# Optimization experiments

Hardware: AMD Instinct MI355X
Metric: run time of the kernel (lower is better)

The kernel has to match this reference:

```python
import jax, jax.numpy as jnp
import numpy as np

B, S, D, H = 2, 2048, 1024, 16
HD = D // H  # head_dim = 64
ROPE_BASE = 10000.0


def setup_inputs() -> dict:
    key = jax.random.key(0)
    ks = jax.random.split(key, 5)
    scale = 1.0 / np.sqrt(D)
    return {
        "x": jax.random.normal(ks[0], (B, S, D), dtype=jnp.float32),
        "Wq": jax.random.normal(ks[1], (D, D), dtype=jnp.float32) * scale,
        "Wk": jax.random.normal(ks[2], (D, D), dtype=jnp.float32) * scale,
        "Wv": jax.random.normal(ks[3], (D, D), dtype=jnp.float32) * scale,
        "Wo": jax.random.normal(ks[4], (D, D), dtype=jnp.float32) * scale,
    }


def _rotate_half(x):
    x1, x2 = x[..., : HD // 2], x[..., HD // 2:]
    return jnp.concatenate((-x2, x1), axis=-1)


def _rope_cos_sin(seq_len):
    inv_freq = 1.0 / (ROPE_BASE ** (jnp.arange(0, HD, 2, dtype=jnp.float32) / HD))
    t = jnp.arange(seq_len, dtype=jnp.float32)
    freqs = jnp.outer(t, inv_freq)          # [S, HD/2]
    emb = jnp.concatenate((freqs, freqs), -1)  # [S, HD]
    return jnp.cos(emb), jnp.sin(emb)


def reference(x, Wq, Wk, Wv, Wo):
    # projections (torch Linear: y = x @ W.T), split heads -> [B, H, S, HD]
    def proj(W):
        return (x @ W.T).reshape(B, S, H, HD).transpose(0, 2, 1, 3)

    q, k, v = proj(Wq), proj(Wk), proj(Wv)

    cos, sin = _rope_cos_sin(S)  # [S, HD] each, broadcast over B, H
    q = q * cos + _rotate_half(q) * sin
    k = k * cos + _rotate_half(k) * sin

    scale = 1.0 / np.sqrt(HD)
    scores = jnp.einsum("bhsd,bhtd->bhst", q, k) * scale  # [B,H,S,S]
    attn = jax.nn.softmax(scores, axis=-1)
    out = jnp.einsum("bhst,bhtd->bhsd", attn, v)           # [B,H,S,HD]
    out = out.transpose(0, 2, 1, 3).reshape(B, S, D)
    return out @ Wo.T
```

## Files before the change

### kernel.cpp

```cpp
#include <hip/hip_runtime.h>
#include <hip/hip_bf16.h>
#include <math.h>
#include <stdint.h>

typedef __bf16 bf16;
typedef __bf16 bf16x8 __attribute__((ext_vector_type(8)));
typedef __bf16 bf16x4 __attribute__((ext_vector_type(4)));
typedef float  f32x4  __attribute__((ext_vector_type(4)));

#define MFMA16(a,b,c) __builtin_amdgcn_mfma_f32_16x16x32_bf16((a),(b),(c),0,0,0)
#define GLOAD_LDS16(g, l) \
  __builtin_amdgcn_global_load_lds((__attribute__((address_space(1))) void*)(g), \
                                   (__attribute__((address_space(3))) void*)(l), 16, 0, 0)

static constexpr int kB  = 2;
static constexpr int kS  = 2048;
static constexpr int kD  = 1024;
static constexpr int kH  = 16;
static constexpr int kHD = 64;
static constexpr int kM  = kB * kS;
static constexpr float kExpC = 0.125f * 1.44269504f;

__global__ void cvt_all(const float* __restrict__ x,
                        const float* __restrict__ wq, const float* __restrict__ wk,
                        const float* __restrict__ wv, const float* __restrict__ wo,
                        bf16* __restrict__ xb,
                        bf16* __restrict__ wqb, bf16* __restrict__ wkb,
                        bf16* __restrict__ wvb, bf16* __restrict__ wob,
                        float2* __restrict__ rtab)
{
  const int i = blockIdx.x * 256 + threadIdx.x;
  const int NX4 = (kM * kD) / 4;
  const int NW4 = (kD * kD) / 4;
  if (i >= NX4 + 4 * NW4) {
    const int idx = i - (NX4 + 4 * NW4);
    const int s = idx >> 5, d = idx & 31;
    const float f = exp2f(-(float)d * 0.4152410118609203f);
    float sn, cs;
    sincosf((float)s * f, &sn, &cs);
    rtab[idx] = make_float2(cs, sn);
    return;
  }
  const float* src; bf16* dst; int off;
  if (i < NX4) { src = x; dst = xb; off = i; }
  else {
    const int j = i - NX4;
    const int seg = j >> 18;
    off = j & (NW4 - 1);
    src = (seg == 0) ? wq : (seg == 1) ? wk : (seg == 2) ? wv : wo;
    dst = (seg == 0) ? wqb : (seg == 1) ? wkb : (seg == 2) ? wvb : wob;
  }
  const float4 v = ((const float4*)src)[off];
  bf16x4 o = { (bf16)v.x, (bf16)v.y, (bf16)v.z, (bf16)v.w };
  ((bf16x4*)dst)[off] = o;
}

__device__ __forceinline__ void gemm_core_128(
    const bf16* __restrict__ A, const bf16* __restrict__ Bw,
    int m0, int n0, int K, bf16* aT, bf16* bT, f32x4 acc[4][4])
{
  const int t = threadIdx.x, lane = t & 63, wave = t >> 6;
  const int wm = wave >> 1, wn = wave & 1;
  const int srow = lane >> 2;
  const int scol = (lane & 3) * 8;
  for (int k0 = 0; k0 < K; k0 += 32) {
    __syncthreads();
#pragma unroll
    for (int c = 0; c < 2; ++c) {
      const int row = c * 64 + wave * 16 + srow;
      const bf16* ga = A  + (size_t)(m0 + row) * K + k0 + scol;
      const bf16* gb = Bw + (size_t)(n0 + row) * K + k0 + scol;
      GLOAD_LDS16(ga, aT + c * 2048 + wave * 512);
      GLOAD_LDS16(gb, bT + c * 2048 + wave * 512);
    }
    __syncthreads();
    bf16x8 af[4], bfr[4];
#pragma unroll
    for (int i = 0; i < 4; ++i) {
      af[i]  = *(const bf16x8*)(aT + (wm * 64 + i * 16 + (lane & 15)) * 32 + (lane >> 4) * 8);
      bfr[i] = *(const bf16x8*)(bT + (wn * 64 + i * 16 + (lane & 15)) * 32 + (lane >> 4) * 8);
    }
#pragma unroll
    for (int i = 0; i < 4; ++i)
#pragma unroll
      for (int j = 0; j < 4; ++j)
        acc[i][j] = MFMA16(af[i], bfr[j], acc[i][j]);
  }
}

__global__ __launch_bounds__(256) void proj_qkv(
    const bf16* __restrict__ xb,
    const bf16* __restrict__ wqb, const bf16* __restrict__ wkb, const bf16* __restrict__ wvb,
    bf16* __restrict__ Qb, bf16* __restrict__ Kb, bf16* __restrict__ Vb,
    const float2* __restrict__ rtab)
{
  __shared__ __align__(16) bf16 aT[4096];
  __shared__ __align__(16) bf16 bT[4096];
  const int z = blockIdx.z;
  const bf16* Ww = (z == 0) ? wqb : (z == 1) ? wkb : wvb;
  bf16*       Op = (z == 0) ? Qb  : (z == 1) ? Kb  : Vb;
  const int m0 = blockIdx.x * 128, n0 = blockIdx.y * 128;
  f32x4 acc[4][4] = {};
  gemm_core_128(xb, Ww, m0, n0, kD, aT, bT, acc);

  const int lane = threadIdx.x & 63, wave = threadIdx.x >> 6;
  const int wm = wave >> 1, wn = wave & 1, quad = lane >> 4, lc = lane & 15;
  const int hh = (n0 >> 6) + wn;
  if (z == 2) {
#pragma unroll
    for (int i = 0; i < 4; ++i)
#pragma unroll
      for (int r = 0; r < 4; ++r) {
        const int m = m0 + wm * 64 + i * 16 + quad * 4 + r;
        const int bidx = m >> 11, s = m & 2047;
        bf16* dst = Op + ((size_t)(bidx * kH + hh) * kS + s) * kHD;
#pragma unroll
        for (int j = 0; j < 4; ++j) dst[j * 16 + lc] = (bf16)acc[i][j][r];
      }
  } else {
    const float f = (z == 0) ? kExpC : 1.0f;
#pragma unroll
    for (int j = 0; j < 2; ++j) {
      const int d = j * 16 + lc;
#pragma unroll
      for (int i = 0; i < 4; ++i)
#pragma unroll
        for (int r = 0; r < 4; ++r) {
          const int m = m0 + wm * 64 + i * 16 + quad * 4 + r;
          const int bidx = m >> 11, s = m & 2047;
          const float2 cs = rtab[s * 32 + d];
          const float v0 = acc[i][j][r], v1 = acc[i][j + 2][r];
          bf16* dst = Op + ((size_t)(bidx * kH + hh) * kS + s) * kHD;
          dst[d]      = (bf16)((v0 * cs.x - v1 * cs.y) * f);
          dst[d + 32] = (bf16)((v1 * cs.x + v0 * cs.y) * f);
        }
    }
  }
}

__global__ __launch_bounds__(256) void transpose_v(
    const bf16* __restrict__ Vb, bf16* __restrict__ Vt)
{
  __shared__ __align__(16) bf16 buf[128 * 72];
  const int t = threadIdx.x;
  const int kc = blockIdx.x, bh = blockIdx.y;
  const bf16* src = Vb + ((size_t)bh * kS + kc * 128) * kHD;
  {
    const int srow = t >> 1, half = (t & 1) * 32;
#pragma unroll
    for (int u = 0; u < 4; ++u)
      *(uint4*)&buf[srow * 72 + half + u * 8] = *(const uint4*)(src + srow * kHD + half + u * 8);
  }
  __syncthreads();
  {
    const int d = t & 63, c = t >> 6;
    bf16 tmp[32];
#pragma unroll
    for (int e = 0; e < 32; ++e) tmp[e] = buf[(c * 32 + e) * 72 + d];
    bf16* dst = Vt + ((size_t)bh * kHD + d) * kS + kc * 128 + c * 32;
#pragma unroll
    for (int u = 0; u < 4; ++u)
      *(uint4*)(dst + u * 8) = *(const uint4*)&tmp[u * 8];
  }
}

__global__ __launch_bounds__(256, 2) void attn(
    const bf16* __restrict__ Qb, const bf16* __restrict__ Kb,
    const bf16* __restrict__ Vt, bf16* __restrict__ Ob)
{
  __shared__ __align__(16) bf16 kT[128 * 72];
  __shared__ __align__(16) bf16 vT[64 * 136];
  __shared__ __align__(16) bf16 pT[4][32 * 136];
  const int t = threadIdx.x, lane = t & 63, wave = t >> 6;
  const int quad = lane >> 4, lc = lane & 15;
  const int qt = blockIdx.x, bh = blockIdx.y;
  const size_t base = (size_t)bh * kS * kHD;
  const bf16* Qp = Qb + base + (size_t)qt * 128 * kHD;
  const bf16* Kp = Kb + base;
  const bf16* Vp = Vt + base;

  bf16x8 qf[2][2];
#pragma unroll
  for (int tm = 0; tm < 2; ++tm)
#pragma unroll
    for (int ks = 0; ks < 2; ++ks)
      qf[tm][ks] = *(const bf16x8*)(Qp + (wave * 32 + tm * 16 + lc) * kHD + ks * 32 + quad * 8);

  f32x4 oacc[2][4] = {};
  f32x4 lacc[2] = {};
  const bf16 one = (bf16)1.0f;
  const bf16x8 ones = { one, one, one, one, one, one, one, one };

  const int srow = t >> 1, shalf = (t & 1) * 32;
  const int vd = t >> 2, vc = t & 3;

  for (int kt = 0; kt < kS / 128; ++kt) {
    __syncthreads();
    {
      const bf16* ksrc = Kp + (size_t)(kt * 128 + srow) * kHD + shalf;
#pragma unroll
      for (int u = 0; u < 4; ++u)
        *(uint4*)&kT[srow * 72 + shalf + u * 8] = *(const uint4*)(ksrc + u * 8);
      const bf16* vsrc = Vp + (size_t)vd * kS + kt * 128 + vc * 32;
#pragma unroll
      for (int u = 0; u < 4; ++u)
        *(uint4*)&vT[vd * 136 + vc * 32 + u * 8] = *(const uint4*)(vsrc + u * 8);
    }
    __syncthreads();

    f32x4 sc[2][8] = {};
#pragma unroll
    for (int nk = 0; nk < 8; ++nk) {
      const bf16x8 kf0 = *(const bf16x8*)&kT[(nk * 16 + lc) * 72 + quad * 8];
      const bf16x8 kf1 = *(const bf16x8*)&kT[(nk * 16 + lc) * 72 + 32 + quad * 8];
#pragma unroll
      for (int tm = 0; tm < 2; ++tm) {
        sc[tm][nk] = MFMA16(kf0, qf[tm][0], sc[tm][nk]);
        sc[tm][nk] = MFMA16(kf1, qf[tm][1], sc[tm][nk]);
      }
    }

    bf16* pw = &pT[wave][0];
#pragma unroll
    for (int tm = 0; tm < 2; ++tm)
#pragma unroll
      for (int nk = 0; nk < 8; ++nk) {
        bf16x4 p;
#pragma unroll
        for (int r = 0; r < 4; ++r)
          p[r] = (bf16)__builtin_amdgcn_exp2f(sc[tm][nk][r]);
        *(bf16x4*)&pw[(tm * 16 + lc) * 136 + nk * 16 + quad * 4] = p;
      }

    bf16x8 pf[2][4];
#pragma unroll
    for (int tm = 0; tm < 2; ++tm)
#pragma unroll
      for (int ks = 0; ks < 4; ++ks)
        pf[tm][ks] = *(const bf16x8*)&pw[(tm * 16 + lc) * 136 + ks * 32 + quad * 8];
#pragma unroll
    for (int ks = 0; ks < 4; ++ks)
#pragma unroll
      for (int tm = 0; tm < 2; ++tm)
        lacc[tm] = MFMA16(pf[tm][ks], ones, lacc[tm]);
#pragma unroll
    for (int nd = 0; nd < 4; ++nd)
#pragma unroll
      for (int ks = 0; ks < 4; ++ks) {
        const bf16x8 vf = *(const bf16x8*)&vT[(nd * 16 + lc) * 136 + ks * 32 + quad * 8];
#pragma unroll
        for (int tm = 0; tm < 2; ++tm)
          oacc[tm][nd] = MFMA16(pf[tm][ks], vf, oacc[tm][nd]);
      }
  }

  const int b = bh >> 4, h = bh & 15;
#pragma unroll
  for (int tm = 0; tm < 2; ++tm)
#pragma unroll
    for (int r = 0; r < 4; ++r) {
      const float inv = 1.0f / lacc[tm][r];
      const int s = qt * 128 + wave * 32 + tm * 16 + quad * 4 + r;
      bf16* dst = Ob + ((size_t)(b * kS + s)) * kD + h * kHD;
#pragma unroll
      for (int nd = 0; nd < 4; ++nd)
        dst[nd * 16 + lc] = (bf16)(oacc[tm][nd][r] * inv);
    }
}

__global__ __launch_bounds__(256) void out_proj(
    const bf16* __restrict__ Ab, const bf16* __restrict__ wob, float* __restrict__ Cout)
{
  __shared__ __align__(16) bf16 aT[4096];
  __shared__ __align__(16) bf16 bT[4096];
  const int m0 = blockIdx.x * 128, n0 = blockIdx.y * 128;
  f32x4 acc[4][4] = {};
  gemm_core_128(Ab, wob, m0, n0, kD, aT, bT, acc);
  const int lane = threadIdx.x & 63, wave = threadIdx.x >> 6;
  const int wm = wave >> 1, wn = wave & 1, quad = lane >> 4, lc = lane & 15;
#pragma unroll
  for (int i = 0; i < 4; ++i)
#pragma unroll
    for (int r = 0; r < 4; ++r) {
      const int m = m0 + wm * 64 + i * 16 + quad * 4 + r;
#pragma unroll
      for (int j = 0; j < 4; ++j)
        Cout[(size_t)m * kD + n0 + wn * 64 + j * 16 + lc] = acc[i][j][r];
    }
}

extern "C" void kernel_launch(void* const* d_in, const int* in_sizes, int n_in,
                              void* d_out, int out_size, void* d_ws, size_t ws_size,
                              hipStream_t stream)
{
  const float* x  = (const float*)d_in[0];
  const float* wq = (const float*)d_in[1];
  const float* wk = (const float*)d_in[2];
  const float* wv = (const float*)d_in[3];
  const float* wo = (const float*)d_in[4];
  float* out = (float*)d_out;

  char* ws = (char*)d_ws;
  const size_t MB = 1024 * 1024;
  if (ws_size < 57 * MB) return;
  bf16* xb  = (bf16*)(ws + 0 * MB);
  bf16* wqb = (bf16*)(ws + 8 * MB);
  bf16* wkb = (bf16*)(ws + 10 * MB);
  bf16* wvb = (bf16*)(ws + 12 * MB);
  bf16* wob = (bf16*)(ws + 14 * MB);
  bf16* Qb  = (bf16*)(ws + 16 * MB);
  bf16* Kb  = (bf16*)(ws + 24 * MB);
  bf16* Vb  = (bf16*)(ws + 32 * MB);
  bf16* Ob  = (bf16*)(ws + 40 * MB);
  float2* rtab = (float2*)(ws + 48 * MB);
  bf16* Vtp = (bf16*)(ws + 49 * MB);

  cvt_all<<<8448, 256, 0, stream>>>(x, wq, wk, wv, wo, xb, wqb, wkb, wvb, wob, rtab);
  proj_qkv<<<dim3(32, 8, 3), 256, 0, stream>>>(xb, wqb, wkb, wvb, Qb, Kb, Vb, rtab);
  transpose_v<<<dim3(16, 32), 256, 0, stream>>>(Vb, Vtp);
  attn<<<dim3(16, 32), 256, 0, stream>>>(Qb, Kb, Vtp, Ob);
  out_proj<<<dim3(32, 8), 256, 0, stream>>>(Ob, wob, out);
}
```

Baseline: 207.4 us.

## Use two waves per attention block with 64 query rows each

The attention kernel now runs 128 threads (2 waves) per block instead of 4, so each wave handles 64 query rows. K fragments are loaded into registers once per tile and reused across four row groups, and each V fragment is reused across four row groups. This cuts LDS reads per MFMA and the cooperative load work per block. The cost is more registers per wave, which with launch bounds (128,1) may lower occupancy, and half as many waves share the same tile loads.

```diff
diff --git a/kernel.cpp b/kernel.cpp
--- a/kernel.cpp
+++ b/kernel.cpp
@@ -164,13 +164,13 @@
   }
 }
 
-__global__ __launch_bounds__(256, 2) void attn(
+__global__ __launch_bounds__(128, 1) void attn(
     const bf16* __restrict__ Qb, const bf16* __restrict__ Kb,
     const bf16* __restrict__ Vt, bf16* __restrict__ Ob)
 {
   __shared__ __align__(16) bf16 kT[128 * 72];
   __shared__ __align__(16) bf16 vT[64 * 136];
-  __shared__ __align__(16) bf16 pT[4][32 * 136];
+  __shared__ __align__(16) bf16 pT[2][64 * 136];
   const int t = threadIdx.x, lane = t & 63, wave = t >> 6;
   const int quad = lane >> 4, lc = lane & 15;
   const int qt = blockIdx.x, bh = blockIdx.y;
@@ -179,88 +179,94 @@
   const bf16* Kp = Kb + base;
   const bf16* Vp = Vt + base;
 
-  bf16x8 qf[2][2];
-#pragma unroll
-  for (int tm = 0; tm < 2; ++tm)
+  bf16x8 qf[4][2];
+#pragma unroll
+  for (int tm = 0; tm < 4; ++tm)
 #pragma unroll
     for (int ks = 0; ks < 2; ++ks)
-      qf[tm][ks] = *(const bf16x8*)(Qp + (wave * 32 + tm * 16 + lc) * kHD + ks * 32 + quad * 8);
-
-  f32x4 oacc[2][4] = {};
-  f32x4 lacc[2] = {};
+      qf[tm][ks] = *(const bf16x8*)(Qp + (wave * 64 + tm * 16 + lc) * kHD + ks * 32 + quad * 8);
+
+  f32x4 oacc[4][4] = {};
+  f32x4 lacc[4] = {};
   const bf16 one = (bf16)1.0f;
   const bf16x8 ones = { one, one, one, one, one, one, one, one };
 
-  const int srow = t >> 1, shalf = (t & 1) * 32;
-  const int vd = t >> 2, vc = t & 3;
+  const int vd = t >> 1, vhalf = (t & 1) * 64;
 
   for (int kt = 0; kt < kS / 128; ++kt) {
     __syncthreads();
     {
-      const bf16* ksrc = Kp + (size_t)(kt * 128 + srow) * kHD + shalf;
-#pragma unroll
-      for (int u = 0; u < 4; ++u)
-        *(uint4*)&kT[srow * 72 + shalf + u * 8] = *(const uint4*)(ksrc + u * 8);
-      const bf16* vsrc = Vp + (size_t)vd * kS + kt * 128 + vc * 32;
-#pragma unroll
-      for (int u = 0; u < 4; ++u)
-        *(uint4*)&vT[vd * 136 + vc * 32 + u * 8] = *(const uint4*)(vsrc + u * 8);
+      const bf16* ksrc = Kp + (size_t)(kt * 128 + t) * kHD;
+#pragma unroll
+      for (int u = 0; u < 8; ++u)
+        *(uint4*)&kT[t * 72 + u * 8] = *(const uint4*)(ksrc + u * 8);
+      const bf16* vsrc = Vp + (size_t)vd * kS + kt * 128 + vhalf;
+#pragma unroll
+      for (int u = 0; u < 8; ++u)
+        *(uint4*)&vT[vd * 136 + vhalf + u * 8] = *(const uint4*)(vsrc + u * 8);
     }
     __syncthreads();
 
-    f32x4 sc[2][8] = {};
-#pragma unroll
-    for (int nk = 0; nk < 8; ++nk) {
-      const bf16x8 kf0 = *(const bf16x8*)&kT[(nk * 16 + lc) * 72 + quad * 8];
-      const bf16x8 kf1 = *(const bf16x8*)&kT[(nk * 16 + lc) * 72 + 32 + quad * 8];
-#pragma unroll
-      for (int tm = 0; tm < 2; ++tm) {
-        sc[tm][nk] = MFMA16(kf0, qf[tm][0], sc[tm][nk]);
-        sc[tm][nk] = MFMA16(kf1, qf[tm][1], sc[tm][nk]);
+    bf16x8 kf[8][2];
+#pragma unroll
+    for (int nk = 0; nk < 8; ++nk)
+#pragma unroll
+      for (int ks = 0; ks < 2; ++ks)
+        kf[nk][ks] = *(const bf16x8*)&kT[(nk * 16 + lc) * 72 + ks * 32 + quad * 8];
+
+    bf16* pw = &pT[wave][0];
+#pragma unroll
+    for (int tm = 0; tm < 4; ++tm) {
+      f32x4 sc[8] = {};
+#pragma unroll
+      for (int nk = 0; nk < 8; ++nk) {
+        sc[nk] = MFMA16(kf[nk][0], qf[tm][0], sc[nk]);
+        sc[nk] = MFMA16(kf[nk][1], qf[tm][1], sc[nk]);
       }
-    }
-
-    bf16* pw = &pT[wave][0];
-#pragma unroll
-    for (int tm = 0; tm < 2; ++tm)
 #pragma unroll
       for (int nk = 0; nk < 8; ++nk) {
         bf16x4 p;
 #pragma unroll
         for (int r = 0; r < 4; ++r)
-          p[r] = (bf16)__builtin_amdgcn_exp2f(sc[tm][nk][r]);
+          p[r] = (bf16)__builtin_amdgcn_exp2f(sc[nk][r]);
         *(bf16x4*)&pw[(tm * 16 + lc) * 136 + nk * 16 + quad * 4] = p;
       }
-
-    bf16x8 pf[2][4];
-#pragma unroll
-    for (int tm = 0; tm < 2; ++tm)
+    }
+
+    bf16x8 pf[4][4];
+#pragma unroll
+    for (int tm = 0; tm < 4; ++tm)
 #pragma unroll
       for (int ks = 0; ks < 4; ++ks)
         pf[tm][ks] = *(const bf16x8*)&pw[(tm * 16 + lc) * 136 + ks * 32 + quad * 8];
+
 #pragma unroll
     for (int ks = 0; ks < 4; ++ks)
 #pragma unroll
-      for (int tm = 0; tm < 2; ++tm)
+      for (int tm = 0; tm < 4; ++tm)
         lacc[tm] = MFMA16(pf[tm][ks], ones, lacc[tm]);
-#pragma unroll
-    for (int nd = 0; nd < 4; ++nd)
-#pragma unroll
-      for (int ks = 0; ks < 4; ++ks) {
-        const bf16x8 vf = *(const bf16x8*)&vT[(nd * 16 + lc) * 136 + ks * 32 + quad * 8];
-#pragma unroll
-        for (int tm = 0; tm < 2; ++tm)
-          oacc[tm][nd] = MFMA16(pf[tm][ks], vf, oacc[tm][nd]);
-      }
+
+#pragma unroll
+    for (int nd = 0; nd < 4; ++nd) {
+      bf16x8 vf[4];
+#pragma unroll
+      for (int ks = 0; ks < 4; ++ks)
+        vf[ks] = *(const bf16x8*)&vT[(nd * 16 + lc) * 136 + ks * 32 + quad * 8];
+#pragma unroll
+      for (int tm = 0; tm < 4; ++tm)
+#pragma unroll
+        for (int ks = 0; ks < 4; ++ks)
+          oacc[tm][nd] = MFMA16(pf[tm][ks], vf[ks], oacc[tm][nd]);
+    }
   }
 
   const int b = bh >> 4, h = bh & 15;
 #pragma unroll
-  for (int tm = 0; tm < 2; ++tm)
+  for (int tm = 0; tm < 4; ++tm)
 #pragma unroll
     for (int r = 0; r < 4; ++r) {
       const float inv = 1.0f / lacc[tm][r];
-      const int s = qt * 128 + wave * 32 + tm * 16 + quad * 4 + r;
+      const int s = qt * 128 + wave * 64 + tm * 16 + quad * 4 + r;
       bf16* dst = Ob + ((size_t)(b * kS + s)) * kD + h * kHD;
 #pragma unroll
       for (int nd = 0; nd < 4; ++nd)
@@ -318,6 +324,6 @@
   cvt_all<<<8448, 256, 0, stream>>>(x, wq, wk, wv, wo, xb, wqb, wkb, wvb, wob, rtab);
   proj_qkv<<<dim3(32, 8, 3), 256, 0, stream>>>(xb, wqb, wkb, wvb, Qb, Kb, Vb, rtab);
   transpose_v<<<dim3(16, 32), 256, 0, stream>>>(Vb, Vtp);
-  attn<<<dim3(16, 32), 256, 0, stream>>>(Qb, Kb, Vtp, Ob);
+  attn<<<dim3(16, 32), 128, 0, stream>>>(Qb, Kb, Vtp, Ob);
   out_proj<<<dim3(32, 8), 256, 0, stream>>>(Ob, wob, out);
 }
```

New measurement: 245.8 us. 1.18x slower.
